# Kernel optimization log

Measured on AMD Instinct MI355X. Metric: run time of the kernel, lower is better.

## Reference

```python
import jax, jax.numpy as jnp
import numpy as np

N_NODES = 20000
N_EDGES = 320000  # directed edges, in reverse pairs (2*i, 2*i+1)
F_NODE = 64
F_EDGE = 16
HID = 300
DEPTH = 3
N_GRAPHS = 128


def setup_inputs() -> dict:
    key = jax.random.key(0)
    ks = jax.random.split(key, 16)
    x = jax.random.normal(ks[0], (N_NODES, F_NODE), dtype=jnp.float32)
    edge_attr = jax.random.normal(ks[1], (N_EDGES, F_EDGE), dtype=jnp.float32)
    # build paired directed edges: edge 2*i is (src,dst), edge 2*i+1 is (dst,src)
    half = N_EDGES // 2
    src = jax.random.randint(ks[2], (half,), 0, N_NODES)
    dst = jax.random.randint(ks[3], (half,), 0, N_NODES)
    row = jnp.stack([src, dst], axis=1).reshape(-1)  # [E]
    col = jnp.stack([dst, src], axis=1).reshape(-1)  # [E]
    edge_index = jnp.stack([row, col], axis=0)  # [2, E]
    batch = jnp.sort(jax.random.randint(ks[4], (N_NODES,), 0, N_GRAPHS))
    s = 0.05
    W_init = jax.random.normal(ks[5], (F_NODE + F_EDGE, HID), dtype=jnp.float32) * s
    b_init = jnp.zeros((HID,), dtype=jnp.float32)
    W_convs = jax.random.normal(ks[6], (DEPTH, HID, HID), dtype=jnp.float32) * s
    b_convs = jnp.zeros((DEPTH, HID), dtype=jnp.float32)
    W_e2n = jax.random.normal(ks[7], (F_NODE + HID, HID), dtype=jnp.float32) * s
    b_e2n = jnp.zeros((HID,), dtype=jnp.float32)
    W_ffn = jax.random.normal(ks[8], (HID, 1), dtype=jnp.float32) * s
    b_ffn = jnp.zeros((1,), dtype=jnp.float32)
    return {"x": x, "edge_attr": edge_attr, "edge_index": edge_index, "batch": batch,
            "W_init": W_init, "b_init": b_init, "W_convs": W_convs, "b_convs": b_convs,
            "W_e2n": W_e2n, "b_e2n": b_e2n, "W_ffn": W_ffn, "b_ffn": b_ffn}


def _rev(h):
    # swap each consecutive forward/reverse edge pair
    e = h.shape[0]
    return h.reshape(e // 2, 2, -1)[:, ::-1, :].reshape(e, -1)


def reference(x, edge_attr, edge_index, batch, W_init, b_init, W_convs, b_convs,
              W_e2n, b_e2n, W_ffn, b_ffn):
    row, col = edge_index[0], edge_index[1]
    # h_0 = act(edge_init(cat([x[row], edge_attr])))
    h0 = jax.nn.relu(jnp.concatenate([x[row], edge_attr], axis=1) @ W_init + b_init)
    h = h0
    for l in range(DEPTH):
        # DMPNNConv: scatter-add edge features to target nodes, gather at source,
        # subtract reverse-edge message, apply Linear
        a = jax.ops.segment_sum(h, col, num_segments=N_NODES)  # [N, H]
        h = (a[row] - _rev(h)) @ W_convs[l] + b_convs[l]
        h = jax.nn.relu(h + h0)  # skip then activation; dropout is eval no-op
    # final conv's a_message only
    s = jax.ops.segment_sum(h, col, num_segments=N_NODES)  # [N, H]
    q = jnp.concatenate([x, s], axis=1)
    hn = jax.nn.relu(q @ W_e2n + b_e2n)  # [N, H]
    pooled = jax.ops.segment_sum(hn, batch, num_segments=N_GRAPHS)  # [G, H]
    return (pooled @ W_ffn + b_ffn).squeeze(-1)  # [G]
```

## Files before the change

### kernel.cpp

```cpp
#include <hip/hip_runtime.h>
#include <hip/hip_bf16.h>

typedef unsigned short ushort_t;
typedef __attribute__((ext_vector_type(8))) short short8;
typedef __attribute__((ext_vector_type(4))) float f32x4;
typedef __attribute__((ext_vector_type(2))) float f32x2;

#define N_NODES 20000
#define N_EDGES 320000
#define F_NODE 64
#define F_EDGE 16
#define HID 300
#define HP 300
#define NTILES 20
#define DEPTH 3
#define N_GRAPHS 128
#define KE2N 384
#define ATS 344

#define WFRAG_USHORT_PER_LAYER (10 * NTILES * 64 * 8)
#define W2FRAG_USHORT (NTILES * 64 * 8)
#define WE2NFRAG_USHORT (12 * NTILES * 64 * 8)

__device__ __forceinline__ float bf2f(ushort_t u) {
    union { unsigned int i; float f; } v;
    v.i = ((unsigned int)u) << 16;
    return v.f;
}

__device__ __forceinline__ f32x2 bfpair(unsigned int u) {
    union { unsigned int i[2]; f32x2 f; } v;
    v.i[0] = u << 16;
    v.i[1] = u & 0xffff0000u;
    return v.f;
}

__device__ __forceinline__ f32x2 pmax0(f32x2 a) {
#if __has_builtin(__builtin_elementwise_max)
    f32x2 z = {0.f, 0.f};
    return __builtin_elementwise_max(a, z);
#else
    f32x2 r; r.x = fmaxf(a.x, 0.f); r.y = fmaxf(a.y, 0.f); return r;
#endif
}

__device__ __forceinline__ unsigned int fpack(float lo, float hi) {
#if __has_builtin(__builtin_amdgcn_cvt_pk_bf16_f32)
    auto r = __builtin_amdgcn_cvt_pk_bf16_f32(lo, hi);
    union { decltype(r) b; unsigned int u; } v;
    v.b = r;
    return v.u;
#else
    union { float f; unsigned int i; } a, b;
    a.f = lo; b.f = hi;
    return ((a.i + 0x8000u) >> 16) | ((b.i + 0x8000u) & 0xffff0000u);
#endif
}
__device__ __forceinline__ unsigned int fpack2(f32x2 a) { return fpack(a.x, a.y); }
__device__ __forceinline__ ushort_t f2bf(float f) {
    return (ushort_t)(fpack(f, 0.f) & 0xffffu);
}

__global__ __launch_bounds__(256) void csr_hist(
    const int* __restrict__ col, int* __restrict__ deg)
{
    int e = blockIdx.x * 256 + threadIdx.x;
    atomicAdd(&deg[col[e]], 1);
}

__global__ __launch_bounds__(256) void csr_scan(
    const int* __restrict__ deg, int* __restrict__ offsets,
    int* __restrict__ cursor)
{
    __shared__ int sums[256];
    const int t = threadIdx.x;
    const int CH = 79;
    int base = t * CH;
    int local = 0;
    for (int i = 0; i < CH; ++i) {
        int idx = base + i;
        if (idx < N_NODES) local += deg[idx];
    }
    sums[t] = local;
    __syncthreads();
    for (int off = 1; off < 256; off <<= 1) {
        int v = (t >= off) ? sums[t - off] : 0;
        __syncthreads();
        sums[t] += v;
        __syncthreads();
    }
    int run = (t > 0) ? sums[t - 1] : 0;
    for (int i = 0; i < CH; ++i) {
        int idx = base + i;
        if (idx < N_NODES) {
            offsets[idx] = run;
            cursor[idx] = run;
            run += deg[idx];
        }
    }
}

__global__ __launch_bounds__(256) void csr_fill(
    const int* __restrict__ col, int* __restrict__ cursor,
    int* __restrict__ eid)
{
    int e = blockIdx.x * 256 + threadIdx.x;
    int pos = atomicAdd(&cursor[col[e]], 1);
    eid[pos] = e;
}

__global__ __launch_bounds__(256) void ghist(
    const int* __restrict__ batch, int* __restrict__ gdeg)
{
    int n = blockIdx.x * 256 + threadIdx.x;
    if (n < N_NODES) atomicAdd(&gdeg[batch[n]], 1);
}

__global__ __launch_bounds__(128) void gscan(
    const int* __restrict__ gdeg, int* __restrict__ goff)
{
    __shared__ int s[128];
    int t = threadIdx.x;
    int d = gdeg[t];
    s[t] = d;
    __syncthreads();
    for (int off = 1; off < 128; off <<= 1) {
        int v = (t >= off) ? s[t - off] : 0;
        __syncthreads();
        s[t] += v;
        __syncthreads();
    }
    goff[t] = s[t] - d;
    if (t == 127) goff[128] = s[127];
}

__global__ __launch_bounds__(64) void wfrag_build(
    const float* __restrict__ W_convs, ushort_t* __restrict__ wfrag)
{
    const int c = blockIdx.x, t = blockIdx.y, l = blockIdx.z;
    const int lane = threadIdx.x;
    const int k0 = c * 32 + (lane >> 4) * 8;
    const int n  = t * 16 + (lane & 15);
    ushort_t* dst = wfrag + (size_t)l * WFRAG_USHORT_PER_LAYER
                  + ((size_t)(c * NTILES + t) * 64 + lane) * 8;
    const float* Wl = W_convs + (size_t)l * HID * HID;
    #pragma unroll
    for (int j = 0; j < 8; ++j) {
        int k = k0 + j;
        float v = (k < HID && n < HID) ? Wl[(long)k * HID + n] : 0.f;
        dst[j] = f2bf(v);
    }
}

__global__ __launch_bounds__(64) void wfrag2_build(
    const float* __restrict__ W_e2n, ushort_t* __restrict__ wfrag2)
{
    const int c = blockIdx.x, t = blockIdx.y;
    const int lane = threadIdx.x;
    const int k0 = c * 32 + (lane >> 4) * 8;
    const int n  = t * 16 + (lane & 15);
    ushort_t* dst = wfrag2 + ((size_t)(c * NTILES + t) * 64 + lane) * 8;
    #pragma unroll
    for (int j = 0; j < 8; ++j) {
        int k = k0 + j;
        float v = (k < F_NODE + HID && n < HID) ? W_e2n[(long)k * HID + n] : 0.f;
        dst[j] = f2bf(v);
    }
}

__global__ __launch_bounds__(64) void w2frag_build(
    const float* __restrict__ W2, ushort_t* __restrict__ w2frag)
{
    const int t = blockIdx.x;
    const int lane = threadIdx.x;
    const int k0 = (lane >> 4) * 8;
    const int n  = t * 16 + (lane & 15);
    ushort_t* dst = w2frag + ((size_t)t * 64 + lane) * 8;
    #pragma unroll
    for (int j = 0; j < 8; ++j) {
        int k = k0 + j;
        float v = (k < F_EDGE && n < HID) ? W2[(long)k * HID + n] : 0.f;
        dst[j] = f2bf(v);
    }
}


__global__ __launch_bounds__(256) void node_init_gemm(
    const float* __restrict__ x, const float* __restrict__ W_init,
    const float* __restrict__ b_init, ushort_t* __restrict__ xW1b)
{
    __shared__ float xs[16 * 64];
    const int tid = threadIdx.x;
    const long n0 = (long)blockIdx.x * 16;
    for (int i = tid; i < 16 * 64; i += 256) xs[i] = x[n0 * 64 + i];
    __syncthreads();
    const int nl = tid >> 4, ct = tid & 15;
    for (int q = 0; q < 19; ++q) {
        int c = ct + 16 * q;
        if (c < HID) {
            float acc = b_init[c];
            #pragma unroll 8
            for (int k = 0; k < 64; ++k)
                acc = fmaf(xs[nl * 64 + k], W_init[(long)k * HID + c], acc);
            xW1b[(n0 + nl) * HID + c] = f2bf(acc);
        }
    }
}

__device__ __forceinline__ void p_phase8(
    ushort_t* At, const float* __restrict__ edge_attr,
    const ushort_t* __restrict__ w2frag, long e0,
    int wave, int quad, int m, int lane)
{
    const int mtp = wave >> 2;
    const int nt0p = (wave & 3) * 5;
    short8 a_ea;
    {
        union { uint4 u4; short8 s8; } af;
        if (quad < 2) {
            const float* eap = edge_attr + (e0 + mtp * 16 + m) * 16 + quad * 8;
            float4 v0 = *(const float4*)eap;
            float4 v1 = *(const float4*)(eap + 4);
            af.u4.x = fpack(v0.x, v0.y); af.u4.y = fpack(v0.z, v0.w);
            af.u4.z = fpack(v1.x, v1.y); af.u4.w = fpack(v1.z, v1.w);
        } else {
            af.u4.x = 0; af.u4.y = 0; af.u4.z = 0; af.u4.w = 0;
        }
        a_ea = af.s8;
    }
    #pragma unroll
    for (int t = 0; t < 5; ++t) {
        int nt = nt0p + t;
        if (nt >= 19) continue;
        short8 b = *(const short8*)(w2frag + ((size_t)nt * 64 + lane) * 8);
        int c = nt * 16 + m;
        f32x4 pc = (f32x4){0.f, 0.f, 0.f, 0.f};
        pc = __builtin_amdgcn_mfma_f32_16x16x32_bf16(a_ea, b, pc, 0, 0, 0);
        #pragma unroll
        for (int r = 0; r < 4; ++r)
            At[(mtp * 16 + quad * 4 + r) * ATS + c] = f2bf(pc[r]);
    }
}

template<bool UPDATE>
__global__ __launch_bounds__(256) void fused_conv(
    ushort_t* h, const ushort_t* __restrict__ Sb,
    const ushort_t* __restrict__ xW1b, const float* __restrict__ edge_attr,
    const int* __restrict__ row, const ushort_t* __restrict__ w2frag,
    const ushort_t* __restrict__ wfrag_l)
{
    __shared__ ushort_t At[32 * ATS];
    __shared__ int rows[32];
    const int tid = threadIdx.x;
    const int wave = tid >> 6, lane = tid & 63;
    const int quad = lane >> 4, m = lane & 15;
    const long e0 = (long)blockIdx.x * 32;
    if (tid < 32) rows[tid] = row[e0 + tid];

    {
        short8 a_ea[2];
        #pragma unroll
        for (int mt = 0; mt < 2; ++mt) {
            union { uint4 u4; short8 s8; } af;
            if (quad < 2) {
                const float* eap = edge_attr + (e0 + mt * 16 + m) * 16 + quad * 8;
                float4 v0 = *(const float4*)eap;
                float4 v1 = *(const float4*)(eap + 4);
                af.u4.x = fpack(v0.x, v0.y); af.u4.y = fpack(v0.z, v0.w);
                af.u4.z = fpack(v1.x, v1.y); af.u4.w = fpack(v1.z, v1.w);
            } else {
                af.u4.x = 0; af.u4.y = 0; af.u4.z = 0; af.u4.w = 0;
            }
            a_ea[mt] = af.s8;
        }
        const int nt0 = wave * 5;
        #pragma unroll
        for (int t = 0; t < 5; ++t) {
            short8 b = *(const short8*)(w2frag + ((size_t)(nt0 + t) * 64 + lane) * 8);
            int c = (nt0 + t) * 16 + m;
            #pragma unroll
            for (int mt = 0; mt < 2; ++mt) {
                f32x4 pc = (f32x4){0.f, 0.f, 0.f, 0.f};
                pc = __builtin_amdgcn_mfma_f32_16x16x32_bf16(a_ea[mt], b, pc, 0, 0, 0);
                #pragma unroll
                for (int r = 0; r < 4; ++r)
                    At[(mt * 16 + quad * 4 + r) * ATS + c] = f2bf(pc[r]);
            }
        }
    }
    __syncthreads();

    for (int i = tid; i < 16 * 80; i += 256) {
        int p = i / 80, g = i % 80;
        int c0 = 4 * g;
        int la = 2 * p, lb = 2 * p + 1;
        uint2 oa, ob;
        if (g < 75) {
            long Ea = e0 + la, Eb = e0 + lb;
            int ra = rows[la], rb = rows[lb];
            uint2 xa = *(const uint2*)&xW1b[(long)ra * HID + c0];
            uint2 xb = *(const uint2*)&xW1b[(long)rb * HID + c0];
            uint2 pa = *(const uint2*)&At[la * ATS + c0];
            uint2 pb = *(const uint2*)&At[lb * ATS + c0];
            f32x2 h0a0 = pmax0(bfpair(xa.x) + bfpair(pa.x));
            f32x2 h0a1 = pmax0(bfpair(xa.y) + bfpair(pa.y));
            f32x2 h0b0 = pmax0(bfpair(xb.x) + bfpair(pb.x));
            f32x2 h0b1 = pmax0(bfpair(xb.y) + bfpair(pb.y));
            if (UPDATE) {
                uint2 wa = *(const uint2*)&h[Ea * HP + c0];
                uint2 wb = *(const uint2*)&h[Eb * HP + c0];
                uint2 sa = *(const uint2*)&Sb[(long)ra * HID + c0];
                uint2 sb = *(const uint2*)&Sb[(long)rb * HID + c0];
                oa.x = fpack2(pmax0(bfpair(sa.x) - bfpair(wb.x) + h0a0));
                oa.y = fpack2(pmax0(bfpair(sa.y) - bfpair(wb.y) + h0a1));
                ob.x = fpack2(pmax0(bfpair(sb.x) - bfpair(wa.x) + h0b0));
                ob.y = fpack2(pmax0(bfpair(sb.y) - bfpair(wa.y) + h0b1));
            } else {
                oa.x = fpack2(h0a0); oa.y = fpack2(h0a1);
                ob.x = fpack2(h0b0); ob.y = fpack2(h0b1);
            }
        } else {
            oa.x = 0; oa.y = 0;
            ob = oa;
        }
        *(uint2*)&At[la * ATS + c0] = oa;
        *(uint2*)&At[lb * ATS + c0] = ob;
    }
    __syncthreads();

    const int nt0 = wave * 5;
    f32x4 acc[5][2];
    #pragma unroll
    for (int t = 0; t < 5; ++t)
        #pragma unroll
        for (int mt = 0; mt < 2; ++mt)
            acc[t][mt] = (f32x4){0.f, 0.f, 0.f, 0.f};

    for (int c = 0; c < 10; ++c) {
        short8 a[2];
        #pragma unroll
        for (int mt = 0; mt < 2; ++mt)
            a[mt] = *(const short8*)&At[(mt * 16 + m) * ATS + c * 32 + quad * 8];
        #pragma unroll
        for (int t = 0; t < 5; ++t) {
            short8 b = *(const short8*)(wfrag_l
                + ((size_t)(c * NTILES + nt0 + t) * 64 + lane) * 8);
            #pragma unroll
            for (int mt = 0; mt < 2; ++mt)
                acc[t][mt] = __builtin_amdgcn_mfma_f32_16x16x32_bf16(
                    a[mt], b, acc[t][mt], 0, 0, 0);
        }
    }
    #pragma unroll
    for (int t = 0; t < 5; ++t) {
        int col = (nt0 + t) * 16 + m;
        if (col >= HID) continue;
        #pragma unroll
        for (int mt = 0; mt < 2; ++mt) {
            long rbase = (e0 + mt * 16 + quad * 4) * HP + col;
            #pragma unroll
            for (int r = 0; r < 4; ++r)
                h[rbase + (long)r * HP] = f2bf(acc[t][mt][r]);
        }
    }
}

__global__ __launch_bounds__(512) void edge_update_mfma(
    ushort_t* h, const ushort_t* __restrict__ Sb,
    const ushort_t* __restrict__ xW1b, const float* __restrict__ edge_attr,
    const int* __restrict__ row, const ushort_t* __restrict__ w2frag)
{
    __shared__ ushort_t Pt[32 * ATS];
    const int tid = threadIdx.x;
    const int wave = tid >> 6, lane = tid & 63;
    const int quad = lane >> 4, m = lane & 15;
    const long e0 = (long)blockIdx.x * 32;

    auto issue = [&](int k, uint2& xa, uint2& xb, uint2& wa, uint2& wb,
                     uint2& sa, uint2& sb, int& la, int& lb, int& g, bool& v) {
        int i = tid + (k << 9);
        v = i < 16 * 75;
        if (v) {
            int p = i / 75; g = i % 75;
            la = 2 * p; lb = la + 1;
            int c0 = 4 * g;
            int ra = row[e0 + la], rb = row[e0 + lb];
            xa = *(const uint2*)&xW1b[(long)ra * HID + c0];
            xb = *(const uint2*)&xW1b[(long)rb * HID + c0];
            wa = *(const uint2*)&h[(e0 + la) * HP + c0];
            wb = *(const uint2*)&h[(e0 + lb) * HP + c0];
            sa = *(const uint2*)&Sb[(long)ra * HID + c0];
            sb = *(const uint2*)&Sb[(long)rb * HID + c0];
        }
    };

    uint2 xa0, xb0, wa0, wb0, sa0, sb0;
    int la0 = 0, lb0 = 0, g0 = 0; bool v0 = false;
    issue(0, xa0, xb0, wa0, wb0, sa0, sb0, la0, lb0, g0, v0);

    p_phase8(Pt, edge_attr, w2frag, e0, wave, quad, m, lane);
    __syncthreads();

    #pragma unroll
    for (int k = 0; k < 3; ++k) {
        uint2 xa1, xb1, wa1, wb1, sa1, sb1;
        int la1 = 0, lb1 = 0, g1 = 0; bool v1 = false;
        if (k < 2)
            issue(k + 1, xa1, xb1, wa1, wb1, sa1, sb1, la1, lb1, g1, v1);
        if (v0) {
            int c0 = 4 * g0;
            uint2 pa = *(const uint2*)&Pt[la0 * ATS + c0];
            uint2 pb = *(const uint2*)&Pt[lb0 * ATS + c0];
            f32x2 h0a0 = pmax0(bfpair(xa0.x) + bfpair(pa.x));
            f32x2 h0a1 = pmax0(bfpair(xa0.y) + bfpair(pa.y));
            f32x2 h0b0 = pmax0(bfpair(xb0.x) + bfpair(pb.x));
            f32x2 h0b1 = pmax0(bfpair(xb0.y) + bfpair(pb.y));
            uint2 oa, ob;
            oa.x = fpack2(pmax0(bfpair(sa0.x) - bfpair(wb0.x) + h0a0));
            oa.y = fpack2(pmax0(bfpair(sa0.y) - bfpair(wb0.y) + h0a1));
            ob.x = fpack2(pmax0(bfpair(sb0.x) - bfpair(wa0.x) + h0b0));
            ob.y = fpack2(pmax0(bfpair(sb0.y) - bfpair(wa0.y) + h0b1));
            *(uint2*)&h[(e0 + la0) * HP + c0] = oa;
            *(uint2*)&h[(e0 + lb0) * HP + c0] = ob;
        }
        if (k < 2) {
            xa0 = xa1; xb0 = xb1; wa0 = wa1; wb0 = wb1;
            sa0 = sa1; sb0 = sb1; la0 = la1; lb0 = lb1; g0 = g1; v0 = v1;
        }
    }
}

__global__ __launch_bounds__(256) void gather_sum(
    const ushort_t* __restrict__ src, const int* __restrict__ offsets,
    const int* __restrict__ ends, const int* __restrict__ eid,
    const float* __restrict__ bias, ushort_t* __restrict__ Sb)
{
    long idx = (long)blockIdx.x * 256 + threadIdx.x;
    if (idx >= (long)N_NODES * 75) return;
    int n = (int)(idx / 75);
    int g = (int)(idx % 75);
    int beg = offsets[n], end = ends[n];
    f32x2 A0 = {0.f, 0.f}, A1 = {0.f, 0.f};
    f32x2 B0 = {0.f, 0.f}, B1 = {0.f, 0.f};
    f32x2 C0 = {0.f, 0.f}, C1 = {0.f, 0.f};
    f32x2 D0 = {0.f, 0.f}, D1 = {0.f, 0.f};
    int j = beg;
    for (; j + 3 < end; j += 4) {
        int ea = eid[j], eb = eid[j + 1], ec = eid[j + 2], ed = eid[j + 3];
        uint2 va = ((const uint2*)src)[(long)ea * (HP / 4) + g];
        uint2 vb = ((const uint2*)src)[(long)eb * (HP / 4) + g];
        uint2 vc = ((const uint2*)src)[(long)ec * (HP / 4) + g];
        uint2 vd = ((const uint2*)src)[(long)ed * (HP / 4) + g];
        A0 += bfpair(va.x); A1 += bfpair(va.y);
        B0 += bfpair(vb.x); B1 += bfpair(vb.y);
        C0 += bfpair(vc.x); C1 += bfpair(vc.y);
        D0 += bfpair(vd.x); D1 += bfpair(vd.y);
    }
    for (; j < end; ++j) {
        int ea = eid[j];
        uint2 va = ((const uint2*)src)[(long)ea * (HP / 4) + g];
        A0 += bfpair(va.x); A1 += bfpair(va.y);
    }
    float4 bv = *(const float4*)&bias[4 * g];
    f32x2 bv0 = {bv.x, bv.y}, bv1 = {bv.z, bv.w};
    uint2 o;
    o.x = fpack2((A0 + B0) + (C0 + D0) + bv0);
    o.y = fpack2((A1 + B1) + (C1 + D1) + bv1);
    *(uint2*)&Sb[(long)n * HID + 4 * g] = o;
}

__global__ __launch_bounds__(256) void gather_ab(
    const ushort_t* __restrict__ src, const int* __restrict__ offsets,
    const int* __restrict__ ends, const int* __restrict__ eid,
    ushort_t* __restrict__ Ab)
{
    long idx = (long)blockIdx.x * 256 + threadIdx.x;
    if (idx >= (long)N_NODES * 75) return;
    int n = (int)(idx / 75);
    int g = (int)(idx % 75);
    int beg = offsets[n], end = ends[n];
    f32x2 A0 = {0.f, 0.f}, A1 = {0.f, 0.f};
    f32x2 B0 = {0.f, 0.f}, B1 = {0.f, 0.f};
    f32x2 C0 = {0.f, 0.f}, C1 = {0.f, 0.f};
    f32x2 D0 = {0.f, 0.f}, D1 = {0.f, 0.f};
    int j = beg;
    for (; j + 3 < end; j += 4) {
        int ea = eid[j], eb = eid[j + 1], ec = eid[j + 2], ed = eid[j + 3];
        uint2 va = ((const uint2*)src)[(long)ea * (HP / 4) + g];
        uint2 vb = ((const uint2*)src)[(long)eb * (HP / 4) + g];
        uint2 vc = ((const uint2*)src)[(long)ec * (HP / 4) + g];
        uint2 vd = ((const uint2*)src)[(long)ed * (HP / 4) + g];
        A0 += bfpair(va.x); A1 += bfpair(va.y);
        B0 += bfpair(vb.x); B1 += bfpair(vb.y);
        C0 += bfpair(vc.x); C1 += bfpair(vc.y);
        D0 += bfpair(vd.x); D1 += bfpair(vd.y);
    }
    for (; j < end; ++j) {
        int ea = eid[j];
        uint2 va = ((const uint2*)src)[(long)ea * (HP / 4) + g];
        A0 += bfpair(va.x); A1 += bfpair(va.y);
    }
    uint2 o;
    o.x = fpack2((A0 + B0) + (C0 + D0));
    o.y = fpack2((A1 + B1) + (C1 + D1));
    *(uint2*)&Ab[(long)n * KE2N + 64 + 4 * g] = o;
}

__global__ __launch_bounds__(256) void x_fill(
    const float* __restrict__ x, ushort_t* __restrict__ Ab)
{
    long idx = (long)blockIdx.x * 256 + threadIdx.x;
    if (idx >= (long)N_NODES * 21) return;
    int n = (int)(idx / 21);
    int q = (int)(idx % 21);
    if (q < 16) {
        float4 v = *(const float4*)&x[(long)n * 64 + 4 * q];
        uint2 o;
        o.x = fpack(v.x, v.y);
        o.y = fpack(v.z, v.w);
        *(uint2*)&Ab[(long)n * KE2N + 4 * q] = o;
    } else {
        uint2 o; o.x = 0; o.y = 0;
        *(uint2*)&Ab[(long)n * KE2N + 364 + 4 * (q - 16)] = o;
    }
}

__global__ __launch_bounds__(256) void e2n_mfma(
    const ushort_t* __restrict__ Ab, const ushort_t* __restrict__ wfrag2,
    const float* __restrict__ b_e2n, float* __restrict__ hn)
{
    const int tid = threadIdx.x;
    const int wave = tid >> 6, lane = tid & 63;
    const int quad = lane >> 4, m = lane & 15;
    const long n0 = (long)blockIdx.x * 32;
    const int nt0 = wave * 5;

    f32x4 acc[5][2];
    #pragma unroll
    for (int t = 0; t < 5; ++t)
        #pragma unroll
        for (int mt = 0; mt < 2; ++mt)
            acc[t][mt] = (f32x4){0.f, 0.f, 0.f, 0.f};

    for (int c = 0; c < 12; ++c) {
        short8 a[2];
        #pragma unroll
        for (int mt = 0; mt < 2; ++mt) {
            long r = n0 + mt * 16 + m;
            a[mt] = *(const short8*)(Ab + r * KE2N + c * 32 + quad * 8);
        }
        #pragma unroll
        for (int t = 0; t < 5; ++t) {
            short8 b = *(const short8*)(wfrag2
                + ((size_t)(c * NTILES + nt0 + t) * 64 + lane) * 8);
            #pragma unroll
            for (int mt = 0; mt < 2; ++mt)
                acc[t][mt] = __builtin_amdgcn_mfma_f32_16x16x32_bf16(
                    a[mt], b, acc[t][mt], 0, 0, 0);
        }
    }

    #pragma unroll
    for (int t = 0; t < 5; ++t) {
        int col = (nt0 + t) * 16 + m;
        if (col >= HID) continue;
        float bias = b_e2n[col];
        #pragma unroll
        for (int mt = 0; mt < 2; ++mt) {
            long rw = n0 + mt * 16 + quad * 4;
            #pragma unroll
            for (int r = 0; r < 4; ++r)
                hn[(rw + r) * HP + col] = fmaxf(acc[t][mt][r] + bias, 0.f);
        }
    }
}

__global__ __launch_bounds__(256) void pool_graph(
    const float* __restrict__ hn, const int* __restrict__ goff,
    float* __restrict__ pooled)
{
    int g = blockIdx.x;
    int beg = goff[g], end = goff[g + 1];
    for (int c = threadIdx.x; c < HID; c += 256) {
        float acc = 0.f;
        for (int n = beg; n < end; ++n)
            acc += hn[(long)n * HP + c];
        pooled[(long)g * HID + c] = acc;
    }
}

__global__ __launch_bounds__(64) void ffn_out(
    const float* __restrict__ pooled, const float* __restrict__ W_ffn,
    const float* __restrict__ b_ffn, float* __restrict__ out)
{
    int g = blockIdx.x;
    int lane = threadIdx.x;
    float s = 0.f;
    for (int c = lane; c < HID; c += 64)
        s += pooled[(long)g * HID + c] * W_ffn[c];
    #pragma unroll
    for (int off = 32; off > 0; off >>= 1)
        s += __shfl_down(s, off, 64);
    if (lane == 0) out[g] = s + b_ffn[0];
}

extern "C" void kernel_launch(void* const* d_in, const int* in_sizes, int n_in,
                              void* d_out, int out_size, void* d_ws, size_t ws_size,
                              hipStream_t stream) {
    const float* x         = (const float*)d_in[0];
    const float* edge_attr = (const float*)d_in[1];
    const int*   edge_index= (const int*)d_in[2];
    const int*   batch     = (const int*)d_in[3];
    const float* W_init    = (const float*)d_in[4];
    const float* b_init    = (const float*)d_in[5];
    const float* W_convs   = (const float*)d_in[6];
    const float* b_convs   = (const float*)d_in[7];
    const float* W_e2n     = (const float*)d_in[8];
    const float* b_e2n     = (const float*)d_in[9];
    const float* W_ffn     = (const float*)d_in[10];
    const float* b_ffn     = (const float*)d_in[11];
    float* out = (float*)d_out;

    const int* row = edge_index;
    const int* col = edge_index + N_EDGES;
    const float* W2 = W_init + (size_t)F_NODE * HID;

    const size_t need = (size_t)N_EDGES * HP * 2
                      + (size_t)N_NODES * HID * 2
                      + (size_t)N_NODES * KE2N * 2
                      + (size_t)N_GRAPHS * HID * 4
                      + (size_t)N_NODES * 4 * 2 + (size_t)N_EDGES * 4
                      + (size_t)DEPTH * WFRAG_USHORT_PER_LAYER * 2
                      + (size_t)WE2NFRAG_USHORT * 2
                      + (size_t)W2FRAG_USHORT * 2
                      + (size_t)(N_GRAPHS + 1 + N_GRAPHS) * 4 + 32768;
    if (ws_size < need) return;

    char* p = (char*)d_ws;
    auto take = [&](size_t bytes) {
        char* q = p;
        p += (bytes + 255) & ~(size_t)255;
        return q;
    };
    ushort_t* h       = (ushort_t*)take((size_t)N_EDGES * HP * 2);
    ushort_t* Sb      = (ushort_t*)take((size_t)N_NODES * HID * 2);
    ushort_t* Ab      = (ushort_t*)take((size_t)N_NODES * KE2N * 2);
    float*    pooled  = (float*)take((size_t)N_GRAPHS * HID * 4);
    int*      cursor  = (int*)take((size_t)N_NODES * 4);
    int*      offsets = (int*)take((size_t)N_NODES * 4);
    int*      eid     = (int*)take((size_t)N_EDGES * 4);
    ushort_t* wfrag   = (ushort_t*)take((size_t)DEPTH * WFRAG_USHORT_PER_LAYER * 2);
    ushort_t* wfrag2  = (ushort_t*)take((size_t)WE2NFRAG_USHORT * 2);
    ushort_t* w2frag  = (ushort_t*)take((size_t)W2FRAG_USHORT * 2);
    int*      gdeg    = (int*)take((size_t)N_GRAPHS * 4);
    int*      goff    = (int*)take((size_t)(N_GRAPHS + 1) * 4);

    ushort_t* xW1b = Ab;
    float*    hn   = (float*)h;

    hipMemsetAsync(cursor, 0, (size_t)N_NODES * 4, stream);
    hipMemsetAsync(gdeg, 0, (size_t)N_GRAPHS * 4, stream);
    csr_hist<<<N_EDGES / 256, 256, 0, stream>>>(col, cursor);
    csr_scan<<<1, 256, 0, stream>>>(cursor, offsets, cursor);
    csr_fill<<<N_EDGES / 256, 256, 0, stream>>>(col, cursor, eid);
    ghist<<<(N_NODES + 255) / 256, 256, 0, stream>>>(batch, gdeg);
    gscan<<<1, 128, 0, stream>>>(gdeg, goff);

    wfrag_build<<<dim3(10, NTILES, DEPTH), 64, 0, stream>>>(W_convs, wfrag);
    wfrag2_build<<<dim3(12, NTILES, 1), 64, 0, stream>>>(W_e2n, wfrag2);
    w2frag_build<<<NTILES, 64, 0, stream>>>(W2, w2frag);

    node_init_gemm<<<N_NODES / 16, 256, 0, stream>>>(x, W_init, b_init, xW1b);

    const int GS_GRID = ((N_NODES * 75) + 255) / 256;

    fused_conv<false><<<N_EDGES / 32, 256, 0, stream>>>(
        h, Sb, xW1b, edge_attr, row, w2frag, wfrag);
    gather_sum<<<GS_GRID, 256, 0, stream>>>(
        h, offsets, cursor, eid, b_convs + 0 * HID, Sb);
    fused_conv<true><<<N_EDGES / 32, 256, 0, stream>>>(
        h, Sb, xW1b, edge_attr, row, w2frag,
        wfrag + 1 * (size_t)WFRAG_USHORT_PER_LAYER);
    gather_sum<<<GS_GRID, 256, 0, stream>>>(
        h, offsets, cursor, eid, b_convs + 1 * HID, Sb);
    fused_conv<true><<<N_EDGES / 32, 256, 0, stream>>>(
        h, Sb, xW1b, edge_attr, row, w2frag,
        wfrag + 2 * (size_t)WFRAG_USHORT_PER_LAYER);
    gather_sum<<<GS_GRID, 256, 0, stream>>>(
        h, offsets, cursor, eid, b_convs + 2 * HID, Sb);
    edge_update_mfma<<<N_EDGES / 32, 512, 0, stream>>>(
        h, Sb, xW1b, edge_attr, row, w2frag);

    x_fill<<<((N_NODES * 21) + 255) / 256, 256, 0, stream>>>(x, Ab);
    gather_ab<<<GS_GRID, 256, 0, stream>>>(h, offsets, cursor, eid, Ab);
    e2n_mfma<<<N_NODES / 32, 256, 0, stream>>>(Ab, wfrag2, b_e2n, hn);
    pool_graph<<<N_GRAPHS, 256, 0, stream>>>(hn, goff, pooled);
    ffn_out<<<N_GRAPHS, 64, 0, stream>>>(pooled, W_ffn, b_ffn, out);
}
```

Measured before the change: 1.211 ms.

## Fuse h0 recompute and message combine into transposed edge-attr MFMA epilogue

The edge-attribute projection MFMA now runs with operands swapped, so each lane holds four consecutive columns of one edge. This lets the h0 relu, the node-sum gather and the reverse-edge subtraction happen directly in registers before a single LDS write. It removes the separate elementwise pass over LDS and one block barrier, and it skips the padding tile 19 in both MFMA loops. In exchange, global gathers now use a per-lane access pattern that may coalesce less well, and the LDS row stride is shrunk.

```diff
diff --git a/kernel.cpp b/kernel.cpp
--- a/kernel.cpp
+++ b/kernel.cpp
@@ -16,10 +16,11 @@
 #define DEPTH 3
 #define N_GRAPHS 128
 #define KE2N 384
-#define ATS 344
+#define ATS 328
 
 #define WFRAG_USHORT_PER_LAYER (10 * NTILES * 64 * 8)
 #define W2FRAG_USHORT (NTILES * 64 * 8)
+#define W2TFRAG_USHORT (19 * 64 * 8)
 #define WE2NFRAG_USHORT (12 * NTILES * 64 * 8)
 
 __device__ __forceinline__ float bf2f(ushort_t u) {
@@ -179,6 +180,23 @@
     #pragma unroll
     for (int j = 0; j < 8; ++j) {
         int k = k0 + j;
+        float v = (k < F_EDGE && n < HID) ? W2[(long)k * HID + n] : 0.f;
+        dst[j] = f2bf(v);
+    }
+}
+
+__global__ __launch_bounds__(64) void w2tfrag_build(
+    const float* __restrict__ W2, ushort_t* __restrict__ w2tfrag)
+{
+    const int t = blockIdx.x;
+    const int lane = threadIdx.x;
+    const int i = lane & 15;
+    const int k0 = (lane >> 4) * 8;
+    ushort_t* dst = w2tfrag + ((size_t)t * 64 + lane) * 8;
+    #pragma unroll
+    for (int j = 0; j < 8; ++j) {
+        int k = k0 + j;
+        int n = t * 16 + i;
         float v = (k < F_EDGE && n < HID) ? W2[(long)k * HID + n] : 0.f;
         dst[j] = f2bf(v);
     }
@@ -246,19 +264,21 @@
 __global__ __launch_bounds__(256) void fused_conv(
     ushort_t* h, const ushort_t* __restrict__ Sb,
     const ushort_t* __restrict__ xW1b, const float* __restrict__ edge_attr,
-    const int* __restrict__ row, const ushort_t* __restrict__ w2frag,
+    const int* __restrict__ row, const ushort_t* __restrict__ w2tfrag,
     const ushort_t* __restrict__ wfrag_l)
 {
     __shared__ ushort_t At[32 * ATS];
-    __shared__ int rows[32];
     const int tid = threadIdx.x;
     const int wave = tid >> 6, lane = tid & 63;
     const int quad = lane >> 4, m = lane & 15;
     const long e0 = (long)blockIdx.x * 32;
-    if (tid < 32) rows[tid] = row[e0 + tid];
+    const int nt0 = wave * 5;
 
     {
-        short8 a_ea[2];
+        int ra0 = row[e0 + m];
+        int ra1 = row[e0 + 16 + m];
+
+        short8 b_ea[2];
         #pragma unroll
         for (int mt = 0; mt < 2; ++mt) {
             union { uint4 u4; short8 s8; } af;
@@ -271,64 +291,48 @@
             } else {
                 af.u4.x = 0; af.u4.y = 0; af.u4.z = 0; af.u4.w = 0;
             }
-            a_ea[mt] = af.s8;
-        }
-        const int nt0 = wave * 5;
+            b_ea[mt] = af.s8;
+        }
+
         #pragma unroll
         for (int t = 0; t < 5; ++t) {
-            short8 b = *(const short8*)(w2frag + ((size_t)(nt0 + t) * 64 + lane) * 8);
-            int c = (nt0 + t) * 16 + m;
+            int nt = nt0 + t;
+            if (nt >= 19) continue;
+            short8 aw = *(const short8*)(w2tfrag + ((size_t)nt * 64 + lane) * 8);
+            int c0 = nt * 16 + quad * 4;
             #pragma unroll
             for (int mt = 0; mt < 2; ++mt) {
+                int el = mt * 16 + m;
+                int ra = mt ? ra1 : ra0;
                 f32x4 pc = (f32x4){0.f, 0.f, 0.f, 0.f};
-                pc = __builtin_amdgcn_mfma_f32_16x16x32_bf16(a_ea[mt], b, pc, 0, 0, 0);
-                #pragma unroll
-                for (int r = 0; r < 4; ++r)
-                    At[(mt * 16 + quad * 4 + r) * ATS + c] = f2bf(pc[r]);
+                pc = __builtin_amdgcn_mfma_f32_16x16x32_bf16(
+                    aw, b_ea[mt], pc, 0, 0, 0);
+                uint2 o;
+                if (c0 < HID) {
+                    uint2 xa = *(const uint2*)&xW1b[(long)ra * HID + c0];
+                    f32x2 h00 = pmax0(bfpair(xa.x) + (f32x2){pc[0], pc[1]});
+                    f32x2 h01 = pmax0(bfpair(xa.y) + (f32x2){pc[2], pc[3]});
+                    if (UPDATE) {
+                        uint2 sa = *(const uint2*)&Sb[(long)ra * HID + c0];
+                        uint2 wv = *(const uint2*)&h[(e0 + (el ^ 1)) * HP + c0];
+                        o.x = fpack2(pmax0(bfpair(sa.x) - bfpair(wv.x) + h00));
+                        o.y = fpack2(pmax0(bfpair(sa.y) - bfpair(wv.y) + h01));
+                    } else {
+                        o.x = fpack2(h00); o.y = fpack2(h01);
+                    }
+                } else {
+                    o.x = 0; o.y = 0;
+                }
+                *(uint2*)&At[el * ATS + c0] = o;
             }
         }
+        if (wave == 3) {
+            int el = lane & 31, half = lane >> 5;
+            *(uint4*)&At[el * ATS + 304 + half * 8] = (uint4){0u, 0u, 0u, 0u};
+        }
     }
     __syncthreads();
 
-    for (int i = tid; i < 16 * 80; i += 256) {
-        int p = i / 80, g = i % 80;
-        int c0 = 4 * g;
-        int la = 2 * p, lb = 2 * p + 1;
-        uint2 oa, ob;
-        if (g < 75) {
-            long Ea = e0 + la, Eb = e0 + lb;
-            int ra = rows[la], rb = rows[lb];
-            uint2 xa = *(const uint2*)&xW1b[(long)ra * HID + c0];
-            uint2 xb = *(const uint2*)&xW1b[(long)rb * HID + c0];
-            uint2 pa = *(const uint2*)&At[la * ATS + c0];
-            uint2 pb = *(const uint2*)&At[lb * ATS + c0];
-            f32x2 h0a0 = pmax0(bfpair(xa.x) + bfpair(pa.x));
-            f32x2 h0a1 = pmax0(bfpair(xa.y) + bfpair(pa.y));
-            f32x2 h0b0 = pmax0(bfpair(xb.x) + bfpair(pb.x));
-            f32x2 h0b1 = pmax0(bfpair(xb.y) + bfpair(pb.y));
-            if (UPDATE) {
-                uint2 wa = *(const uint2*)&h[Ea * HP + c0];
-                uint2 wb = *(const uint2*)&h[Eb * HP + c0];
-                uint2 sa = *(const uint2*)&Sb[(long)ra * HID + c0];
-                uint2 sb = *(const uint2*)&Sb[(long)rb * HID + c0];
-                oa.x = fpack2(pmax0(bfpair(sa.x) - bfpair(wb.x) + h0a0));
-                oa.y = fpack2(pmax0(bfpair(sa.y) - bfpair(wb.y) + h0a1));
-                ob.x = fpack2(pmax0(bfpair(sb.x) - bfpair(wa.x) + h0b0));
-                ob.y = fpack2(pmax0(bfpair(sb.y) - bfpair(wa.y) + h0b1));
-            } else {
-                oa.x = fpack2(h0a0); oa.y = fpack2(h0a1);
-                ob.x = fpack2(h0b0); ob.y = fpack2(h0b1);
-            }
-        } else {
-            oa.x = 0; oa.y = 0;
-            ob = oa;
-        }
-        *(uint2*)&At[la * ATS + c0] = oa;
-        *(uint2*)&At[lb * ATS + c0] = ob;
-    }
-    __syncthreads();
-
-    const int nt0 = wave * 5;
     f32x4 acc[5][2];
     #pragma unroll
     for (int t = 0; t < 5; ++t)
@@ -343,6 +347,7 @@
             a[mt] = *(const short8*)&At[(mt * 16 + m) * ATS + c * 32 + quad * 8];
         #pragma unroll
         for (int t = 0; t < 5; ++t) {
+            if (nt0 + t >= 19) continue;
             short8 b = *(const short8*)(wfrag_l
                 + ((size_t)(c * NTILES + nt0 + t) * 64 + lane) * 8);
             #pragma unroll
@@ -633,6 +638,7 @@
                       + (size_t)DEPTH * WFRAG_USHORT_PER_LAYER * 2
                       + (size_t)WE2NFRAG_USHORT * 2
                       + (size_t)W2FRAG_USHORT * 2
+                      + (size_t)W2TFRAG_USHORT * 2
                       + (size_t)(N_GRAPHS + 1 + N_GRAPHS) * 4 + 32768;
     if (ws_size < need) return;
 
@@ -652,6 +658,7 @@
     ushort_t* wfrag   = (ushort_t*)take((size_t)DEPTH * WFRAG_USHORT_PER_LAYER * 2);
     ushort_t* wfrag2  = (ushort_t*)take((size_t)WE2NFRAG_USHORT * 2);
     ushort_t* w2frag  = (ushort_t*)take((size_t)W2FRAG_USHORT * 2);
+    ushort_t* w2tfrag = (ushort_t*)take((size_t)W2TFRAG_USHORT * 2);
     int*      gdeg    = (int*)take((size_t)N_GRAPHS * 4);
     int*      goff    = (int*)take((size_t)(N_GRAPHS + 1) * 4);
 
@@ -669,22 +676,23 @@
     wfrag_build<<<dim3(10, NTILES, DEPTH), 64, 0, stream>>>(W_convs, wfrag);
     wfrag2_build<<<dim3(12, NTILES, 1), 64, 0, stream>>>(W_e2n, wfrag2);
     w2frag_build<<<NTILES, 64, 0, stream>>>(W2, w2frag);
+    w2tfrag_build<<<19, 64, 0, stream>>>(W2, w2tfrag);
 
     node_init_gemm<<<N_NODES / 16, 256, 0, stream>>>(x, W_init, b_init, xW1b);
 
     const int GS_GRID = ((N_NODES * 75) + 255) / 256;
 
     fused_conv<false><<<N_EDGES / 32, 256, 0, stream>>>(
-        h, Sb, xW1b, edge_attr, row, w2frag, wfrag);
+        h, Sb, xW1b, edge_attr, row, w2tfrag, wfrag);
     gather_sum<<<GS_GRID, 256, 0, stream>>>(
         h, offsets, cursor, eid, b_convs + 0 * HID, Sb);
     fused_conv<true><<<N_EDGES / 32, 256, 0, stream>>>(
-        h, Sb, xW1b, edge_attr, row, w2frag,
+        h, Sb, xW1b, edge_attr, row, w2tfrag,
         wfrag + 1 * (size_t)WFRAG_USHORT_PER_LAYER);
     gather_sum<<<GS_GRID, 256, 0, stream>>>(
         h, offsets, cursor, eid, b_convs + 1 * HID, Sb);
     fused_conv<true><<<N_EDGES / 32, 256, 0, stream>>>(
-        h, Sb, xW1b, edge_attr, row, w2frag,
+        h, Sb, xW1b, edge_attr, row, w2tfrag,
         wfrag + 2 * (size_t)WFRAG_USHORT_PER_LAYER);
     gather_sum<<<GS_GRID, 256, 0, stream>>>(
         h, offsets, cursor, eid, b_convs + 2 * HID, Sb);
```

New measurement: 1.608 ms. 1.33x slower.
